# Kernel optimization log

Measured on AMD Instinct MI355X. Metric: run time of the kernel, lower is better.

The kernel has to match this reference:

```python
import jax, jax.numpy as jnp
import numpy as np

N = 32768
E = 524288
NFEAT = 256
NHID = 256
NUM_HEADS = 4
HEAD_DIM = NHID // NUM_HEADS
NLAYER = 2
EPS = 1e-5


def setup_inputs():
    keys = iter(jax.random.split(jax.random.key(0), 64))

    def nrm(shape, scale=0.05):
        return jax.random.normal(next(keys), shape, dtype=jnp.float32) * scale

    inp = {
        "x": jax.random.normal(next(keys), (N, NFEAT), dtype=jnp.float32),
        "edge_src": jax.random.randint(next(keys), (E,), 0, N),
        "edge_dst": jax.random.randint(next(keys), (E,), 0, N),
        "edge_attr": jax.random.uniform(next(keys), (E,), dtype=jnp.float32) * 0.1,
        "num_graphs": 64,
    }
    for i in range(NLAYER):
        fin = NFEAT if i == 0 else NHID
        inp["conv_w%d" % i] = nrm((fin, NHID))
        inp["bn_g%d" % i] = jnp.ones((NHID,), jnp.float32)
        inp["bn_b%d" % i] = jnp.zeros((NHID,), jnp.float32)
        inp["bn_m%d" % i] = nrm((NHID,), 0.1)
        inp["bn_v%d" % i] = 1.0 + jax.random.uniform(next(keys), (NHID,), dtype=jnp.float32) * 0.1
        inp["attn_in_w%d" % i] = nrm((3 * NHID, NHID))
        inp["attn_in_b%d" % i] = jnp.zeros((3 * NHID,), jnp.float32)
        inp["attn_out_w%d" % i] = nrm((NHID, NHID))
        inp["attn_out_b%d" % i] = jnp.zeros((NHID,), jnp.float32)
        inp["ln_g%d" % i] = jnp.ones((NHID,), jnp.float32)
        inp["ln_b%d" % i] = jnp.zeros((NHID,), jnp.float32)
    inp["score_w"] = nrm((1, NHID))
    inp["score_b"] = jnp.zeros((1,), jnp.float32)
    return inp


def _mha(xb, iw, ib, ow, ob):
    # torch.nn.MultiheadAttention (batch_first), all graphs same length so
    # key_padding_mask is all-False (no masked positions).
    B, S, H = xb.shape
    q, k, v = jnp.split(xb @ iw.T + ib, 3, axis=-1)
    heads = lambda t: t.reshape(B, S, NUM_HEADS, HEAD_DIM).transpose(0, 2, 1, 3)
    q, k, v = heads(q), heads(k), heads(v)
    scale = jnp.float32(1.0 / np.sqrt(HEAD_DIM))
    att = jax.nn.softmax(jnp.einsum("bhqd,bhkd->bhqk", q, k) * scale, axis=-1)
    o = jnp.einsum("bhqk,bhkd->bhqd", att, v).transpose(0, 2, 1, 3).reshape(B, S, H)
    return o @ ow.T + ob


def _forward(x, edge_attr, params, edge_src, edge_dst, num_graphs):
    n = x.shape[0]
    B = num_graphs
    S = n // B  # equal-sized graphs -> max_nodes == S, pad is a no-op
    h = x
    for i, (cw, bng, bnb, bnm, bnv, iw, ib, ow, ob, lg, lb) in enumerate(params):
        # DIGCNConv: out[dst] += edge_attr * (x @ W)[src]
        conv = jax.ops.segment_sum(edge_attr[:, None] * (h @ cw)[edge_src], edge_dst, num_segments=n)
        # BatchNorm1d (eval mode, running stats)
        conv = (conv - bnm) * jax.lax.rsqrt(bnv + EPS) * bng + bnb
        # ragged gather -> pad/stack -> MHA -> unpad (equal graph sizes => reshape)
        attended = _mha(conv.reshape(B, S, NHID), iw, ib, ow, ob).reshape(n, NHID)
        y = conv + attended
        mu = jnp.mean(y, axis=-1, keepdims=True)
        var = jnp.mean((y - mu) ** 2, axis=-1, keepdims=True)
        h = (y - mu) * jax.lax.rsqrt(var + EPS) * lg + lb  # LayerNorm
        if i < NLAYER - 1:
            h = jax.nn.relu(h)
    return h


def reference(x, edge_src, edge_dst, edge_attr, num_graphs,
              conv_w0, bn_g0, bn_b0, bn_m0, bn_v0, attn_in_w0, attn_in_b0, attn_out_w0, attn_out_b0, ln_g0, ln_b0,
              conv_w1, bn_g1, bn_b1, bn_m1, bn_v1, attn_in_w1, attn_in_b1, attn_out_w1, attn_out_b1, ln_g1, ln_b1,
              score_w, score_b):
    params = [
        (conv_w0, bn_g0, bn_b0, bn_m0, bn_v0, attn_in_w0, attn_in_b0, attn_out_w0, attn_out_b0, ln_g0, ln_b0),
        (conv_w1, bn_g1, bn_b1, bn_m1, bn_v1, attn_in_w1, attn_in_b1, attn_out_w1, attn_out_b1, ln_g1, ln_b1),
    ]
    h = _forward(x, edge_attr, params, edge_src, edge_dst, num_graphs)
    scores = (h @ score_w.T + score_b)[:, 0]
    # emb_list / score_list are per-graph views of these flat arrays
    return h, scores
```

## Files before the change

kernel.cpp:

```cpp
#include <hip/hip_runtime.h>
#include <hip/hip_bf16.h>
#include <math.h>

#define N_NODES 32768
#define E_EDGES 524288
#define NHID    256
#define HEAD_DIM 64
#define SEQ     512
#define EPS_LN  1e-5f
#define SM_SCALE 0.18033688011112042f

typedef __hip_bfloat16 bf16;
typedef __attribute__((ext_vector_type(8))) short short8;
typedef __attribute__((ext_vector_type(4))) float floatx4;
static const size_t NH = (size_t)N_NODES * NHID;

__device__ __forceinline__ void unpack2(unsigned int u, float& lo, float& hi) {
    union { float f; unsigned int i; } a, b;
    a.i = u << 16; b.i = u & 0xffff0000u;
    lo = a.f; hi = b.f;
}

__device__ __forceinline__ void* swzp(void* base, int row, int col) {
    return (char*)base + (((row << 7) + (col << 1)) ^ ((row & 7) << 4));
}

__device__ __forceinline__ void gload16(const bf16* g, void* lds) {
    __builtin_amdgcn_global_load_lds((const __attribute__((address_space(1))) void*)g,
                                     (__attribute__((address_space(3))) void*)lds, 16, 0, 0);
}

__global__ void k_cvtb4(bf16* __restrict__ dst, const float* __restrict__ src) {
    size_t i = (size_t)(blockIdx.x * 256 + threadIdx.x) * 4;
    const float4 v = *(const float4*)(src + i);
    __align__(8) bf16 tmp[4];
    tmp[0] = __float2bfloat16(v.x);
    tmp[1] = __float2bfloat16(v.y);
    tmp[2] = __float2bfloat16(v.z);
    tmp[3] = __float2bfloat16(v.w);
    *(uint2*)(dst + i) = *(uint2*)tmp;
}

__global__ __launch_bounds__(256) void k_stage(const float* __restrict__ cw,
                                               const float* __restrict__ bng,
                                               const float* __restrict__ bnb,
                                               const float* __restrict__ bnm,
                                               const float* __restrict__ bnv,
                                               const float* __restrict__ iw,
                                               const float* __restrict__ ow,
                                               bf16* __restrict__ iwb,
                                               bf16* __restrict__ owb,
                                               bf16* __restrict__ cwT,
                                               float* __restrict__ bns,
                                               float* __restrict__ bnt) {
    const int blk = blockIdx.x;
    const int tid = threadIdx.x;
    if (blk < 256) {
        const float* src = (blk < 192) ? iw : ow;
        bf16* dst = (blk < 192) ? iwb : owb;
        size_t i = (size_t)((blk < 192 ? blk : blk - 192) * 256 + tid) * 4;
        const float4 v = *(const float4*)(src + i);
        __align__(8) bf16 t4[4];
        t4[0] = __float2bfloat16(v.x);
        t4[1] = __float2bfloat16(v.y);
        t4[2] = __float2bfloat16(v.z);
        t4[3] = __float2bfloat16(v.w);
        *(uint2*)(dst + i) = *(uint2*)t4;
    } else if (blk < 512) {
        const int k = blk - 256;
        cwT[(size_t)tid * 256 + k] = __float2bfloat16(cw[(size_t)k * 256 + tid]);
    } else {
        float sv = bng[tid] * rsqrtf(bnv[tid] + EPS_LN);
        bns[tid] = sv;
        bnt[tid] = bnb[tid] - bnm[tid] * sv;
    }
}

__global__ void k_hist(const int* __restrict__ edst, int* __restrict__ counts) {
    int e = blockIdx.x * 256 + threadIdx.x;
    atomicAdd(&counts[edst[e]], 1);
}

__global__ __launch_bounds__(256) void k_scan(const int* __restrict__ counts,
                                              int* __restrict__ offsets,
                                              int* __restrict__ cursor) {
    __shared__ int sums[256];
    const int tid = threadIdx.x;
    const int base = tid * 128;
    int s = 0;
    for (int i = 0; i < 128; ++i) s += counts[base + i];
    sums[tid] = s;
    __syncthreads();
    for (int off = 1; off < 256; off <<= 1) {
        int v = (tid >= off) ? sums[tid - off] : 0;
        __syncthreads();
        sums[tid] += v;
        __syncthreads();
    }
    int run = (tid == 0) ? 0 : sums[tid - 1];
    for (int i = 0; i < 128; ++i) {
        int c = counts[base + i];
        offsets[base + i] = run;
        cursor[base + i] = run;
        run += c;
    }
    if (tid == 255) offsets[32768] = run;
}

__global__ void k_fill(const int* __restrict__ esrc, const int* __restrict__ edst,
                       const float* __restrict__ eattr, int* __restrict__ cursor,
                       int* __restrict__ srcp, float* __restrict__ attrp) {
    int e = blockIdx.x * 256 + threadIdx.x;
    int d = edst[e];
    int slot = atomicAdd(&cursor[d], 1);
    srcp[slot] = esrc[e];
    attrp[slot] = eattr[e];
}

__global__ __launch_bounds__(256) void k_gather(const bf16* __restrict__ t,
                                                const int* __restrict__ offsets,
                                                const int* __restrict__ srcp,
                                                const float* __restrict__ attrp,
                                                const float* __restrict__ bns,
                                                const float* __restrict__ bnt,
                                                bf16* __restrict__ conv) {
    const int node = (blockIdx.x * 256 + threadIdx.x) >> 6;
    const int lane = threadIdx.x & 63;
    const int start = offsets[node];
    const int end = offsets[node + 1];
    float a0 = 0.f, a1 = 0.f, a2 = 0.f, a3 = 0.f;
    for (int c0 = start; c0 < end; c0 += 64) {
        const int n = min(64, end - c0);
        int sidx = 0;
        float sa = 0.f;
        if (lane < n) {
            sidx = srcp[c0 + lane];
            sa = attrp[c0 + lane];
        }
        for (int j = 0; j < n; ++j) {
            const int s = __shfl(sidx, j, 64);
            const float a = __shfl(sa, j, 64);
            uint2 u = *(const uint2*)(t + (size_t)s * 256 + lane * 4);
            float v0, v1, v2, v3;
            unpack2(u.x, v0, v1);
            unpack2(u.y, v2, v3);
            a0 = fmaf(a, v0, a0);
            a1 = fmaf(a, v1, a1);
            a2 = fmaf(a, v2, a2);
            a3 = fmaf(a, v3, a3);
        }
    }
    const int c = lane * 4;
    const float4 sv = *(const float4*)(bns + c);
    const float4 tv = *(const float4*)(bnt + c);
    __align__(8) bf16 tmp[4];
    tmp[0] = __float2bfloat16(fmaf(a0, sv.x, tv.x));
    tmp[1] = __float2bfloat16(fmaf(a1, sv.y, tv.y));
    tmp[2] = __float2bfloat16(fmaf(a2, sv.z, tv.z));
    tmp[3] = __float2bfloat16(fmaf(a3, sv.w, tv.w));
    *(uint2*)(conv + (size_t)node * 256 + c) = *(uint2*)tmp;
}

__global__ __launch_bounds__(256) void k_gemm(const bf16* __restrict__ A,
                                              const bf16* __restrict__ WT,
                                              const float* __restrict__ bias,
                                              bf16* __restrict__ C, int ldc, int qscale) {
    __shared__ __align__(16) short As[128 * 64];
    __shared__ __align__(16) short Bs[128 * 64];
    const int tid = threadIdx.x;
    const int bm = blockIdx.x * 128;
    const int bn = blockIdx.y * 128;
    const int wid = tid >> 6;
    const int lane = tid & 63;
    const int wr = (wid >> 1) * 64;
    const int wc = (wid & 1) * 64;
    const int quad = lane >> 4;
    const int l16 = lane & 15;

    floatx4 acc[4][4];
#pragma unroll
    for (int mi = 0; mi < 4; ++mi)
#pragma unroll
        for (int ni = 0; ni < 4; ++ni)
            acc[mi][ni] = (floatx4){0.f, 0.f, 0.f, 0.f};

    for (int k0 = 0; k0 < 256; k0 += 64) {
#pragma unroll
        for (int t = 0; t < 4; ++t) {
            const int p = ((t * 4 + wid) << 10) + (lane << 4);
            const int row = p >> 7;
            const int cb = (p & 127) ^ ((row & 7) << 4);
            gload16(A + (size_t)(bm + row) * 256 + k0 + (cb >> 1),
                    (char*)As + ((t * 4 + wid) << 10));
            gload16(WT + (size_t)(bn + row) * 256 + k0 + (cb >> 1),
                    (char*)Bs + ((t * 4 + wid) << 10));
        }
        __syncthreads();
#pragma unroll
        for (int kk = 0; kk < 2; ++kk) {
            const int kcol = kk * 32 + quad * 8;
            short8 af[4], bfr[4];
#pragma unroll
            for (int mi = 0; mi < 4; ++mi)
                af[mi] = *(const short8*)swzp(As, wr + mi * 16 + l16, kcol);
#pragma unroll
            for (int ni = 0; ni < 4; ++ni)
                bfr[ni] = *(const short8*)swzp(Bs, wc + ni * 16 + l16, kcol);
#pragma unroll
            for (int mi = 0; mi < 4; ++mi)
#pragma unroll
                for (int ni = 0; ni < 4; ++ni)
                    acc[mi][ni] = __builtin_amdgcn_mfma_f32_16x16x32_bf16(af[mi], bfr[ni],
                                                                          acc[mi][ni], 0, 0, 0);
        }
        __syncthreads();
    }
    const float cs = (qscale && bn < 256) ? SM_SCALE : 1.0f;
#pragma unroll
    for (int ni = 0; ni < 4; ++ni) {
        const int gc = bn + wc + ni * 16 + l16;
        const float bv = bias ? bias[gc] : 0.f;
#pragma unroll
        for (int mi = 0; mi < 4; ++mi) {
            const int gr = bm + wr + mi * 16 + quad * 4;
#pragma unroll
            for (int r = 0; r < 4; ++r)
                C[(size_t)(gr + r) * ldc + gc] = __float2bfloat16((acc[mi][ni][r] + bv) * cs);
        }
    }
}

__global__ __launch_bounds__(256) void k_vtrans(const bf16* __restrict__ qkv,
                                                bf16* __restrict__ vtb) {
    const int st = blockIdx.x & 7;
    const int head = (blockIdx.x >> 3) & 3;
    const int b = blockIdx.x >> 5;
    const int tid = threadIdx.x;
    __shared__ __align__(16) short T[64][72];
    const int r = tid >> 3;
    const int c = (tid & 7) * 8;
#pragma unroll
    for (int p = 0; p < 2; ++p) {
        const int s = r + p * 32;
        *(uint4*)&T[s][c] =
            *(const uint4*)(qkv + (size_t)(b * SEQ + st * 64 + s) * 768 + 512 + head * 64 + c);
    }
    __syncthreads();
#pragma unroll
    for (int p = 0; p < 2; ++p) {
        const int d = r + p * 32;
        __align__(16) bf16 tmp[8];
#pragma unroll
        for (int j = 0; j < 8; ++j) tmp[j] = *(const bf16*)&T[c + j][d];
        *(uint4*)(vtb + (size_t)((b * 4 + head) * 64 + d) * 512 + st * 64 + c) = *(uint4*)tmp;
    }
}

__global__ __launch_bounds__(256) void k_fattn(const bf16* __restrict__ qkv,
                                               const bf16* __restrict__ vtb,
                                               bf16* __restrict__ ctx) {
    const int bid = ((blockIdx.x & 7) << 8) | (blockIdx.x >> 3);
    const int qt = bid & 7;
    const int head = (bid >> 3) & 3;
    const int b = bid >> 5;
    const int tid = threadIdx.x;
    const int wave = tid >> 6;
    const int lane = tid & 63;
    const int quad = lane >> 4;
    const int l16 = lane & 15;
    const int qrow0 = b * SEQ + qt * 64 + wave * 16;

    __shared__ __align__(16) short Ks[2][64 * 64];
    __shared__ __align__(16) short Vt[2][64 * 64];
    __shared__ __align__(16) short Ps[4][16 * 64];

    const bf16* kbase = qkv + (size_t)(b * SEQ) * 768 + 256 + head * HEAD_DIM;
    const bf16* vbase = vtb + (size_t)((b * 4 + head) * 64) * 512;
    const int pbase = (wave << 10) + (lane << 4);

    short8 af_q[2];
    {
        const bf16* qp = qkv + (size_t)(qrow0 + l16) * 768 + head * HEAD_DIM + quad * 8;
        af_q[0] = *(const short8*)(qp);
        af_q[1] = *(const short8*)(qp + 32);
    }
    short8 ones;
#pragma unroll
    for (int j = 0; j < 8; ++j) ones[j] = (short)0x3F80;

    floatx4 acc[5];
#pragma unroll
    for (int nt = 0; nt < 5; ++nt) acc[nt] = (floatx4){0.f, 0.f, 0.f, 0.f};

    auto STAGE = [&](int kt2, int bf) {
#pragma unroll
        for (int i = 0; i < 2; ++i) {
            const int p = (i << 12) + pbase;
            const int row = p >> 7;
            const int cb = (p & 127) ^ ((row & 7) << 4);
            gload16(kbase + (size_t)(kt2 * 64 + row) * 768 + (cb >> 1),
                    (char*)Ks[bf] + (i << 12) + (wave << 10));
            gload16(vbase + (size_t)row * 512 + kt2 * 64 + (cb >> 1),
                    (char*)Vt[bf] + (i << 12) + (wave << 10));
        }
    };

    STAGE(0, 0);
    __syncthreads();

    for (int kt = 0; kt < 8; ++kt) {
        const int buf = kt & 1;
        if (kt < 7) STAGE(kt + 1, buf ^ 1);

        floatx4 sf[4];
#pragma unroll
        for (int f = 0; f < 4; ++f) {
            const short8 bk0 = *(const short8*)swzp(Ks[buf], f * 16 + l16, quad * 8);
            const short8 bk1 = *(const short8*)swzp(Ks[buf], f * 16 + l16, 32 + quad * 8);
            sf[f] = __builtin_amdgcn_mfma_f32_16x16x32_bf16(af_q[0], bk0,
                                                            (floatx4){0.f, 0.f, 0.f, 0.f}, 0, 0, 0);
            sf[f] = __builtin_amdgcn_mfma_f32_16x16x32_bf16(af_q[1], bk1, sf[f], 0, 0, 0);
        }

        bf16* psb = (bf16*)&Ps[wave][0];
#pragma unroll
        for (int r = 0; r < 4; ++r) {
            const float p0 = exp2f(fminf(sf[0][r], 80.f));
            const float p1 = exp2f(fminf(sf[1][r], 80.f));
            const float p2 = exp2f(fminf(sf[2][r], 80.f));
            const float p3 = exp2f(fminf(sf[3][r], 80.f));
            const int qr = quad * 4 + r;
            *(bf16*)swzp(psb, qr, l16)      = __float2bfloat16(p0);
            *(bf16*)swzp(psb, qr, 16 + l16) = __float2bfloat16(p1);
            *(bf16*)swzp(psb, qr, 32 + l16) = __float2bfloat16(p2);
            *(bf16*)swzp(psb, qr, 48 + l16) = __float2bfloat16(p3);
        }

#pragma unroll
        for (int c2 = 0; c2 < 2; ++c2) {
            const short8 ap = *(const short8*)swzp(psb, l16, c2 * 32 + quad * 8);
#pragma unroll
            for (int nt = 0; nt < 4; ++nt) {
                const short8 bv = *(const short8*)swzp(Vt[buf], nt * 16 + l16, c2 * 32 + quad * 8);
                acc[nt] = __builtin_amdgcn_mfma_f32_16x16x32_bf16(ap, bv, acc[nt], 0, 0, 0);
            }
            acc[4] = __builtin_amdgcn_mfma_f32_16x16x32_bf16(ap, ones, acc[4], 0, 0, 0);
        }
        __syncthreads();
    }

#pragma unroll
    for (int r = 0; r < 4; ++r) {
        const float inv = 1.f / acc[4][r];
        bf16* op = ctx + (size_t)(qrow0 + quad * 4 + r) * 256 + head * HEAD_DIM + l16;
        op[0]  = __float2bfloat16(acc[0][r] * inv);
        op[16] = __float2bfloat16(acc[1][r] * inv);
        op[32] = __float2bfloat16(acc[2][r] * inv);
        op[48] = __float2bfloat16(acc[3][r] * inv);
    }
}

__global__ void k_ln(const bf16* __restrict__ conv, const bf16* __restrict__ proj,
                     const float* __restrict__ lg, const float* __restrict__ lb,
                     bf16* __restrict__ h, int relu) {
    int gt = blockIdx.x * blockDim.x + threadIdx.x;
    int node = gt >> 6;
    int lane = gt & 63;
    size_t base = (size_t)node * 256 + lane * 4;
    uint2 ua = *(const uint2*)(conv + base);
    uint2 up = *(const uint2*)(proj + base);
    float a0, a1, a2, a3, p0, p1, p2, p3;
    unpack2(ua.x, a0, a1);
    unpack2(ua.y, a2, a3);
    unpack2(up.x, p0, p1);
    unpack2(up.y, p2, p3);
    float y0 = a0 + p0, y1 = a1 + p1, y2 = a2 + p2, y3 = a3 + p3;
    float sum = y0 + y1 + y2 + y3;
#pragma unroll
    for (int off = 32; off > 0; off >>= 1) sum += __shfl_xor(sum, off, 64);
    float mu = sum * (1.0f / 256.0f);
    float d0 = y0 - mu, d1 = y1 - mu, d2 = y2 - mu, d3 = y3 - mu;
    float vs = d0 * d0 + d1 * d1 + d2 * d2 + d3 * d3;
#pragma unroll
    for (int off = 32; off > 0; off >>= 1) vs += __shfl_xor(vs, off, 64);
    float r = rsqrtf(vs * (1.0f / 256.0f) + EPS_LN);
    int c = lane * 4;
    float o0 = fmaf(d0 * r, lg[c + 0], lb[c + 0]);
    float o1 = fmaf(d1 * r, lg[c + 1], lb[c + 1]);
    float o2 = fmaf(d2 * r, lg[c + 2], lb[c + 2]);
    float o3 = fmaf(d3 * r, lg[c + 3], lb[c + 3]);
    if (relu) {
        o0 = fmaxf(o0, 0.f); o1 = fmaxf(o1, 0.f); o2 = fmaxf(o2, 0.f); o3 = fmaxf(o3, 0.f);
    }
    __align__(8) bf16 tmp[4];
    tmp[0] = __float2bfloat16(o0);
    tmp[1] = __float2bfloat16(o1);
    tmp[2] = __float2bfloat16(o2);
    tmp[3] = __float2bfloat16(o3);
    *(uint2*)(h + base) = *(uint2*)tmp;
}

__global__ void k_out(const bf16* __restrict__ h, const float* __restrict__ sw,
                      const float* __restrict__ sb, float* __restrict__ out) {
    int gt = blockIdx.x * blockDim.x + threadIdx.x;
    int node = gt >> 6;
    int lane = gt & 63;
    size_t base = (size_t)node * 256 + lane * 4;
    uint2 uh = *(const uint2*)(h + base);
    float v0, v1, v2, v3;
    unpack2(uh.x, v0, v1);
    unpack2(uh.y, v2, v3);
    *(float4*)(out + base) = make_float4(v0, v1, v2, v3);
    int c = lane * 4;
    float part = v0 * sw[c + 0] + v1 * sw[c + 1] + v2 * sw[c + 2] + v3 * sw[c + 3];
#pragma unroll
    for (int off = 32; off > 0; off >>= 1) part += __shfl_xor(part, off, 64);
    if (lane == 0)
        out[(size_t)N_NODES * 256 + node] = part + sb[0];
}

extern "C" void kernel_launch(void* const* d_in, const int* in_sizes, int n_in,
                              void* d_out, int out_size, void* d_ws, size_t ws_size,
                              hipStream_t stream) {
    if (ws_size < (size_t)100663296) return;

    const float* x     = (const float*)d_in[0];
    const int*   esrc  = (const int*)d_in[1];
    const int*   edst  = (const int*)d_in[2];
    const float* eattr = (const float*)d_in[3];

    bf16* convb = (bf16*)d_ws;
    bf16* qkvb  = convb + NH;
    bf16* tb    = qkvb + 3 * NH;
    bf16* vtb   = tb + NH;
    bf16* xb  = qkvb;
    bf16* hb  = qkvb + NH;
    bf16* pjb = qkvb;

    char* scr = (char*)d_out;
    const size_t LBYTES = 393216 + 131072 + 131072 + 2048;
    int*   counts  = (int*)(scr + 2 * LBYTES);
    int*   offsets = counts + 32768;
    int*   cursor  = offsets + 32769;
    int*   srcp    = cursor + 32768;
    float* attrp   = (float*)(srcp + E_EDGES);

    (void)hipMemsetAsync(counts, 0, 32768 * sizeof(int), stream);
    k_hist<<<E_EDGES / 256, 256, 0, stream>>>(edst, counts);
    k_scan<<<1, 256, 0, stream>>>(counts, offsets, cursor);
    k_fill<<<E_EDGES / 256, 256, 0, stream>>>(esrc, edst, eattr, cursor, srcp, attrp);

    for (int L = 0; L < 2; ++L) {
        int bi = 5 + L * 11;
        char* base = scr + (size_t)L * LBYTES;
        bf16*  iwb = (bf16*)base;
        bf16*  owb = iwb + 196608;
        bf16*  cwT = owb + 65536;
        float* bns = (float*)(cwT + 65536);
        float* bnt = bns + 256;
        k_stage<<<513, 256, 0, stream>>>((const float*)d_in[bi + 0], (const float*)d_in[bi + 1],
                                         (const float*)d_in[bi + 2], (const float*)d_in[bi + 3],
                                         (const float*)d_in[bi + 4], (const float*)d_in[bi + 5],
                                         (const float*)d_in[bi + 7], iwb, owb, cwT, bns, bnt);
    }

    k_cvtb4<<<8192, 256, 0, stream>>>(xb, x);

    for (int L = 0; L < 2; ++L) {
        int bi = 5 + L * 11;
        char* base = scr + (size_t)L * LBYTES;
        bf16*  iwb = (bf16*)base;
        bf16*  owb = iwb + 196608;
        bf16*  cwT = owb + 65536;
        float* bns = (float*)(cwT + 65536);
        float* bnt = bns + 256;
        const float* ib = (const float*)d_in[bi + 6];
        const float* ob = (const float*)d_in[bi + 8];

        k_gemm<<<dim3(256, 2), 256, 0, stream>>>(L == 0 ? xb : hb, cwT, nullptr, tb, 256, 0);
        k_gather<<<8192, 256, 0, stream>>>(tb, offsets, srcp, attrp, bns, bnt, convb);
        k_gemm<<<dim3(256, 6), 256, 0, stream>>>(convb, iwb, ib, qkvb, 768, 1);
        k_vtrans<<<2048, 256, 0, stream>>>(qkvb, vtb);
        k_fattn<<<2048, 256, 0, stream>>>(qkvb, vtb, tb);
        k_gemm<<<dim3(256, 2), 256, 0, stream>>>(tb, owb, ob, pjb, 256, 0);
        k_ln<<<8192, 256, 0, stream>>>(convb, pjb, (const float*)d_in[bi + 9],
                                       (const float*)d_in[bi + 10], hb, L == 0 ? 1 : 0);
    }

    k_out<<<8192, 256, 0, stream>>>(hb, (const float*)d_in[27], (const float*)d_in[28],
                                    (float*)d_out);
}
```

Before: 550.4 us.

## Fuse V transpose into QKV GEMM, fuse final LN with output, widen gather

The QKV GEMM epilogue now writes the V columns directly in transposed per-head layout, which removes the separate k_vtrans kernel. The last layer's LayerNorm is fused with the score projection and fp32 output write, which drops one round trip of h through memory and one launch. The gather now has each half-wave process a different edge and load 16-byte rows, then combines the two halves with a shuffle. The attention MFMA sections are also wrapped in s_setprio raises. The transposed V stores in the GEMM are strided 8-byte writes, which may coalesce poorly.

```diff
diff --git a/kernel.cpp b/kernel.cpp
--- a/kernel.cpp
+++ b/kernel.cpp
@@ -126,9 +126,13 @@
                                                 bf16* __restrict__ conv) {
     const int node = (blockIdx.x * 256 + threadIdx.x) >> 6;
     const int lane = threadIdx.x & 63;
+    const int half = lane >> 5;
+    const int l32 = lane & 31;
     const int start = offsets[node];
     const int end = offsets[node + 1];
-    float a0 = 0.f, a1 = 0.f, a2 = 0.f, a3 = 0.f;
+    float a[8];
+#pragma unroll
+    for (int i = 0; i < 8; ++i) a[i] = 0.f;
     for (int c0 = start; c0 < end; c0 += 64) {
         const int n = min(64, end - c0);
         int sidx = 0;
@@ -137,34 +141,52 @@
             sidx = srcp[c0 + lane];
             sa = attrp[c0 + lane];
         }
-        for (int j = 0; j < n; ++j) {
-            const int s = __shfl(sidx, j, 64);
-            const float a = __shfl(sa, j, 64);
-            uint2 u = *(const uint2*)(t + (size_t)s * 256 + lane * 4);
-            float v0, v1, v2, v3;
+        for (int j = 0; j < n; j += 2) {
+            const int e = j + half;
+            const int s = __shfl(sidx, e, 64);
+            const float aw = __shfl(sa, e, 64);
+            const uint4 u = *(const uint4*)(t + (size_t)s * 256 + l32 * 8);
+            float v0, v1, v2, v3, v4, v5, v6, v7;
             unpack2(u.x, v0, v1);
             unpack2(u.y, v2, v3);
-            a0 = fmaf(a, v0, a0);
-            a1 = fmaf(a, v1, a1);
-            a2 = fmaf(a, v2, a2);
-            a3 = fmaf(a, v3, a3);
-        }
-    }
-    const int c = lane * 4;
-    const float4 sv = *(const float4*)(bns + c);
-    const float4 tv = *(const float4*)(bnt + c);
-    __align__(8) bf16 tmp[4];
-    tmp[0] = __float2bfloat16(fmaf(a0, sv.x, tv.x));
-    tmp[1] = __float2bfloat16(fmaf(a1, sv.y, tv.y));
-    tmp[2] = __float2bfloat16(fmaf(a2, sv.z, tv.z));
-    tmp[3] = __float2bfloat16(fmaf(a3, sv.w, tv.w));
-    *(uint2*)(conv + (size_t)node * 256 + c) = *(uint2*)tmp;
+            unpack2(u.z, v4, v5);
+            unpack2(u.w, v6, v7);
+            a[0] = fmaf(aw, v0, a[0]);
+            a[1] = fmaf(aw, v1, a[1]);
+            a[2] = fmaf(aw, v2, a[2]);
+            a[3] = fmaf(aw, v3, a[3]);
+            a[4] = fmaf(aw, v4, a[4]);
+            a[5] = fmaf(aw, v5, a[5]);
+            a[6] = fmaf(aw, v6, a[6]);
+            a[7] = fmaf(aw, v7, a[7]);
+        }
+    }
+#pragma unroll
+    for (int i = 0; i < 8; ++i) a[i] += __shfl_xor(a[i], 32, 64);
+    if (half == 0) {
+        const int c = l32 * 8;
+        const float4 s0 = *(const float4*)(bns + c);
+        const float4 s1 = *(const float4*)(bns + c + 4);
+        const float4 t0 = *(const float4*)(bnt + c);
+        const float4 t1 = *(const float4*)(bnt + c + 4);
+        __align__(16) bf16 tmp[8];
+        tmp[0] = __float2bfloat16(fmaf(a[0], s0.x, t0.x));
+        tmp[1] = __float2bfloat16(fmaf(a[1], s0.y, t0.y));
+        tmp[2] = __float2bfloat16(fmaf(a[2], s0.z, t0.z));
+        tmp[3] = __float2bfloat16(fmaf(a[3], s0.w, t0.w));
+        tmp[4] = __float2bfloat16(fmaf(a[4], s1.x, t1.x));
+        tmp[5] = __float2bfloat16(fmaf(a[5], s1.y, t1.y));
+        tmp[6] = __float2bfloat16(fmaf(a[6], s1.z, t1.z));
+        tmp[7] = __float2bfloat16(fmaf(a[7], s1.w, t1.w));
+        *(uint4*)(conv + (size_t)node * 256 + c) = *(uint4*)tmp;
+    }
 }
 
 __global__ __launch_bounds__(256) void k_gemm(const bf16* __restrict__ A,
                                               const bf16* __restrict__ WT,
                                               const float* __restrict__ bias,
-                                              bf16* __restrict__ C, int ldc, int qscale) {
+                                              bf16* __restrict__ C, bf16* __restrict__ VT,
+                                              int ldc, int qkvmode) {
     __shared__ __align__(16) short As[128 * 64];
     __shared__ __align__(16) short Bs[128 * 64];
     const int tid = threadIdx.x;
@@ -215,7 +237,8 @@
         }
         __syncthreads();
     }
-    const float cs = (qscale && bn < 256) ? SM_SCALE : 1.0f;
+    const float cs = (qkvmode && bn < 256) ? SM_SCALE : 1.0f;
+    const bool vpath = (qkvmode && bn >= 512);
 #pragma unroll
     for (int ni = 0; ni < 4; ++ni) {
         const int gc = bn + wc + ni * 16 + l16;
@@ -223,36 +246,21 @@
 #pragma unroll
         for (int mi = 0; mi < 4; ++mi) {
             const int gr = bm + wr + mi * 16 + quad * 4;
-#pragma unroll
-            for (int r = 0; r < 4; ++r)
-                C[(size_t)(gr + r) * ldc + gc] = __float2bfloat16((acc[mi][ni][r] + bv) * cs);
-        }
-    }
-}
-
-__global__ __launch_bounds__(256) void k_vtrans(const bf16* __restrict__ qkv,
-                                                bf16* __restrict__ vtb) {
-    const int st = blockIdx.x & 7;
-    const int head = (blockIdx.x >> 3) & 3;
-    const int b = blockIdx.x >> 5;
-    const int tid = threadIdx.x;
-    __shared__ __align__(16) short T[64][72];
-    const int r = tid >> 3;
-    const int c = (tid & 7) * 8;
-#pragma unroll
-    for (int p = 0; p < 2; ++p) {
-        const int s = r + p * 32;
-        *(uint4*)&T[s][c] =
-            *(const uint4*)(qkv + (size_t)(b * SEQ + st * 64 + s) * 768 + 512 + head * 64 + c);
-    }
-    __syncthreads();
-#pragma unroll
-    for (int p = 0; p < 2; ++p) {
-        const int d = r + p * 32;
-        __align__(16) bf16 tmp[8];
-#pragma unroll
-        for (int j = 0; j < 8; ++j) tmp[j] = *(const bf16*)&T[c + j][d];
-        *(uint4*)(vtb + (size_t)((b * 4 + head) * 64 + d) * 512 + st * 64 + c) = *(uint4*)tmp;
+            if (vpath) {
+                const int head = (gc - 512) >> 6;
+                const int d = (gc - 512) & 63;
+                const int bg = gr >> 9;
+                const int sl = gr & 511;
+                __align__(8) bf16 t4[4];
+#pragma unroll
+                for (int r = 0; r < 4; ++r) t4[r] = __float2bfloat16(acc[mi][ni][r] + bv);
+                *(uint2*)(VT + (((size_t)((bg * 4 + head) * 64 + d)) << 9) + sl) = *(uint2*)t4;
+            } else {
+#pragma unroll
+                for (int r = 0; r < 4; ++r)
+                    C[(size_t)(gr + r) * ldc + gc] = __float2bfloat16((acc[mi][ni][r] + bv) * cs);
+            }
+        }
     }
 }
 
@@ -313,6 +321,7 @@
         if (kt < 7) STAGE(kt + 1, buf ^ 1);
 
         floatx4 sf[4];
+        __builtin_amdgcn_s_setprio(1);
 #pragma unroll
         for (int f = 0; f < 4; ++f) {
             const short8 bk0 = *(const short8*)swzp(Ks[buf], f * 16 + l16, quad * 8);
@@ -321,6 +330,7 @@
                                                             (floatx4){0.f, 0.f, 0.f, 0.f}, 0, 0, 0);
             sf[f] = __builtin_amdgcn_mfma_f32_16x16x32_bf16(af_q[1], bk1, sf[f], 0, 0, 0);
         }
+        __builtin_amdgcn_s_setprio(0);
 
         bf16* psb = (bf16*)&Ps[wave][0];
 #pragma unroll
@@ -336,6 +346,7 @@
             *(bf16*)swzp(psb, qr, 48 + l16) = __float2bfloat16(p3);
         }
 
+        __builtin_amdgcn_s_setprio(1);
 #pragma unroll
         for (int c2 = 0; c2 < 2; ++c2) {
             const short8 ap = *(const short8*)swzp(psb, l16, c2 * 32 + quad * 8);
@@ -346,6 +357,7 @@
             }
             acc[4] = __builtin_amdgcn_mfma_f32_16x16x32_bf16(ap, ones, acc[4], 0, 0, 0);
         }
+        __builtin_amdgcn_s_setprio(0);
         __syncthreads();
     }
 
@@ -362,7 +374,7 @@
 
 __global__ void k_ln(const bf16* __restrict__ conv, const bf16* __restrict__ proj,
                      const float* __restrict__ lg, const float* __restrict__ lb,
-                     bf16* __restrict__ h, int relu) {
+                     bf16* __restrict__ h) {
     int gt = blockIdx.x * blockDim.x + threadIdx.x;
     int node = gt >> 6;
     int lane = gt & 63;
@@ -385,13 +397,10 @@
     for (int off = 32; off > 0; off >>= 1) vs += __shfl_xor(vs, off, 64);
     float r = rsqrtf(vs * (1.0f / 256.0f) + EPS_LN);
     int c = lane * 4;
-    float o0 = fmaf(d0 * r, lg[c + 0], lb[c + 0]);
-    float o1 = fmaf(d1 * r, lg[c + 1], lb[c + 1]);
-    float o2 = fmaf(d2 * r, lg[c + 2], lb[c + 2]);
-    float o3 = fmaf(d3 * r, lg[c + 3], lb[c + 3]);
-    if (relu) {
-        o0 = fmaxf(o0, 0.f); o1 = fmaxf(o1, 0.f); o2 = fmaxf(o2, 0.f); o3 = fmaxf(o3, 0.f);
-    }
+    float o0 = fmaxf(fmaf(d0 * r, lg[c + 0], lb[c + 0]), 0.f);
+    float o1 = fmaxf(fmaf(d1 * r, lg[c + 1], lb[c + 1]), 0.f);
+    float o2 = fmaxf(fmaf(d2 * r, lg[c + 2], lb[c + 2]), 0.f);
+    float o3 = fmaxf(fmaf(d3 * r, lg[c + 3], lb[c + 3]), 0.f);
     __align__(8) bf16 tmp[4];
     tmp[0] = __float2bfloat16(o0);
     tmp[1] = __float2bfloat16(o1);
@@ -400,19 +409,38 @@
     *(uint2*)(h + base) = *(uint2*)tmp;
 }
 
-__global__ void k_out(const bf16* __restrict__ h, const float* __restrict__ sw,
-                      const float* __restrict__ sb, float* __restrict__ out) {
+__global__ void k_lnout(const bf16* __restrict__ conv, const bf16* __restrict__ proj,
+                        const float* __restrict__ lg, const float* __restrict__ lb,
+                        const float* __restrict__ sw, const float* __restrict__ sb,
+                        float* __restrict__ out) {
     int gt = blockIdx.x * blockDim.x + threadIdx.x;
     int node = gt >> 6;
     int lane = gt & 63;
     size_t base = (size_t)node * 256 + lane * 4;
-    uint2 uh = *(const uint2*)(h + base);
-    float v0, v1, v2, v3;
-    unpack2(uh.x, v0, v1);
-    unpack2(uh.y, v2, v3);
-    *(float4*)(out + base) = make_float4(v0, v1, v2, v3);
+    uint2 ua = *(const uint2*)(conv + base);
+    uint2 up = *(const uint2*)(proj + base);
+    float a0, a1, a2, a3, p0, p1, p2, p3;
+    unpack2(ua.x, a0, a1);
+    unpack2(ua.y, a2, a3);
+    unpack2(up.x, p0, p1);
+    unpack2(up.y, p2, p3);
+    float y0 = a0 + p0, y1 = a1 + p1, y2 = a2 + p2, y3 = a3 + p3;
+    float sum = y0 + y1 + y2 + y3;
+#pragma unroll
+    for (int off = 32; off > 0; off >>= 1) sum += __shfl_xor(sum, off, 64);
+    float mu = sum * (1.0f / 256.0f);
+    float d0 = y0 - mu, d1 = y1 - mu, d2 = y2 - mu, d3 = y3 - mu;
+    float vs = d0 * d0 + d1 * d1 + d2 * d2 + d3 * d3;
+#pragma unroll
+    for (int off = 32; off > 0; off >>= 1) vs += __shfl_xor(vs, off, 64);
+    float r = rsqrtf(vs * (1.0f / 256.0f) + EPS_LN);
     int c = lane * 4;
-    float part = v0 * sw[c + 0] + v1 * sw[c + 1] + v2 * sw[c + 2] + v3 * sw[c + 3];
+    float o0 = fmaf(d0 * r, lg[c + 0], lb[c + 0]);
+    float o1 = fmaf(d1 * r, lg[c + 1], lb[c + 1]);
+    float o2 = fmaf(d2 * r, lg[c + 2], lb[c + 2]);
+    float o3 = fmaf(d3 * r, lg[c + 3], lb[c + 3]);
+    *(float4*)(out + base) = make_float4(o0, o1, o2, o3);
+    float part = o0 * sw[c + 0] + o1 * sw[c + 1] + o2 * sw[c + 2] + o3 * sw[c + 3];
 #pragma unroll
     for (int off = 32; off > 0; off >>= 1) part += __shfl_xor(part, off, 64);
     if (lane == 0)
@@ -477,16 +505,20 @@
         const float* ib = (const float*)d_in[bi + 6];
         const float* ob = (const float*)d_in[bi + 8];
 
-        k_gemm<<<dim3(256, 2), 256, 0, stream>>>(L == 0 ? xb : hb, cwT, nullptr, tb, 256, 0);
+        k_gemm<<<dim3(256, 2), 256, 0, stream>>>(L == 0 ? xb : hb, cwT, nullptr, tb, nullptr,
+                                                 256, 0);
         k_gather<<<8192, 256, 0, stream>>>(tb, offsets, srcp, attrp, bns, bnt, convb);
-        k_gemm<<<dim3(256, 6), 256, 0, stream>>>(convb, iwb, ib, qkvb, 768, 1);
-        k_vtrans<<<2048, 256, 0, stream>>>(qkvb, vtb);
+        k_gemm<<<dim3(256, 6), 256, 0, stream>>>(convb, iwb, ib, qkvb, vtb, 768, 1);
         k_fattn<<<2048, 256, 0, stream>>>(qkvb, vtb, tb);
-        k_gemm<<<dim3(256, 2), 256, 0, stream>>>(tb, owb, ob, pjb, 256, 0);
-        k_ln<<<8192, 256, 0, stream>>>(convb, pjb, (const float*)d_in[bi + 9],
-                                       (const float*)d_in[bi + 10], hb, L == 0 ? 1 : 0);
-    }
-
-    k_out<<<8192, 256, 0, stream>>>(hb, (const float*)d_in[27], (const float*)d_in[28],
-                                    (float*)d_out);
-}
+        k_gemm<<<dim3(256, 2), 256, 0, stream>>>(tb, owb, ob, pjb, nullptr, 256, 0);
+        if (L == 0) {
+            k_ln<<<8192, 256, 0, stream>>>(convb, pjb, (const float*)d_in[bi + 9],
+                                           (const float*)d_in[bi + 10], hb);
+        } else {
+            k_lnout<<<8192, 256, 0, stream>>>(convb, pjb, (const float*)d_in[bi + 9],
+                                              (const float*)d_in[bi + 10],
+                                              (const float*)d_in[27], (const float*)d_in[28],
+                                              (float*)d_out);
+        }
+    }
+}
```

Result: faster. 523.3 us (-4.9%).
